# Kernel tuning notes

Hardware: AMD Instinct MI355X
Metric: run time of the kernel (lower is better)

## Reference

```python
import jax, jax.numpy as jnp
import numpy as np

B, DIM, H, W = 64, 640, 10, 10
EPS = 1e-05


def setup_inputs() -> dict:
    key = jax.random.key(0)
    k1, _ = jax.random.split(key)
    x = jax.random.normal(k1, (B, DIM, H, W), dtype=jnp.float32)
    init_temp = 1.0 / (2 * H * W)
    temperature = jnp.log(init_temp * jnp.ones((1, 1), dtype=jnp.float32))
    return {"x": x, "temperature": temperature}


def reference(x, temperature):
    b, d, h, w = x.shape
    xf = x.reshape(b, d, h * w)                       # [B, d, n]
    gram = jnp.einsum('bdn,ben->bde', xf, xf)         # [B, d, d]
    diag = jnp.diagonal(gram, axis1=1, axis2=2)       # [B, d]
    # ones @ (gram*eye) == diag[None,:]; (gram*eye) @ ones == diag[:,None]
    dcov = diag[:, :, None] + diag[:, None, :] - 2.0 * gram
    dcov = jnp.sqrt(jnp.exp(temperature[0, 0]) * jnp.clip(dcov, 0.0) + EPS)
    # double-centering: ones-matmuls are row/col/total means scaled by d
    row = jnp.mean(dcov, axis=2, keepdims=True)       # dcov @ ones / d
    col = jnp.mean(dcov, axis=1, keepdims=True)       # ones @ dcov / d
    tot = jnp.mean(dcov, axis=(1, 2), keepdims=True)  # ones @ dcov @ ones / d^2
    centered = dcov - row - col + tot                 # [B, d, d]
    iu = jnp.triu_indices(d)
    return centered[:, iu[0], iu[1]]                  # [B, d*(d+1)/2]
```

## Files before the change

kernel.cpp:

```cpp
#include <hip/hip_runtime.h>
#include <hip/hip_bf16.h>

#define B_    64
#define DIM   640
#define TS    64
#define NT    10
#define TRI   205120
#define EPS   1e-5f
#define SQEPS 3.1622776601683794e-3f
#define KCH   16
#define TILE_U4 1024
#define TILE_B  16384

typedef __attribute__((ext_vector_type(8)))  short bf16x8;
typedef __attribute__((ext_vector_type(16))) float f32x16;

__device__ inline unsigned pk_bf16(float a, float b) {
    __hip_bfloat162 h = __float22bfloat162_rn(float2{a, b});
    return *reinterpret_cast<unsigned*>(&h);
}
__device__ inline float bsq(unsigned pk) {
    union { unsigned u; float f; } a, c;
    a.u = pk << 16;
    c.u = pk & 0xffff0000u;
    return a.f * a.f + c.f * c.f;
}
__device__ inline float fsq(float x) { return __builtin_amdgcn_sqrtf(x); }

__device__ inline void gload_lds16(const void* g, void* l) {
    __builtin_amdgcn_global_load_lds(
        (const __attribute__((address_space(1))) unsigned*)g,
        (__attribute__((address_space(3))) unsigned*)l, 16, 0, 0);
}
__device__ inline void stage_tile16(const char* __restrict__ gt, char* lt,
                                    int wv, int lane) {
    #pragma unroll
    for (int it = 0; it < 4; ++it) {
        const int seg = (wv * 4 + it) * 1024;
        gload_lds16(gt + seg + lane * 16, lt + seg);
    }
}

__global__ __launch_bounds__(256) void prep_kernel(
    const float* __restrict__ x, uint4* __restrict__ img,
    float* __restrict__ dsq)
{
    const int blk = blockIdx.x;
    const int b = blk / NT, s = blk % NT;
    const int t = threadIdx.x;
    const float4* src = (const float4*)x + (size_t)(b * DIM + s * TS) * 25;
    uint4* dst = img + (size_t)blk * TILE_U4;

    #pragma unroll
    for (int ff = 0; ff < 4; ++ff) {
        const int f = t + ff * 256;
        const int r = f >> 4, c = f & 15;
        uint4 p = {0u, 0u, 0u, 0u};
        float sq = 0.f;
        if (c <= 12) {
            float4 lo = src[(size_t)r * 25 + 2 * c];
            float4 hi = make_float4(0.f, 0.f, 0.f, 0.f);
            if (c < 12) hi = src[(size_t)r * 25 + 2 * c + 1];
            p.x = pk_bf16(lo.x, lo.y);
            p.y = pk_bf16(lo.z, lo.w);
            p.z = pk_bf16(hi.x, hi.y);
            p.w = pk_bf16(hi.z, hi.w);
            sq = bsq(p.x) + bsq(p.y) + bsq(p.z) + bsq(p.w);
        }
        dst[r * KCH + (c ^ (r & 15))] = p;
        sq += __shfl_xor(sq, 1);
        sq += __shfl_xor(sq, 2);
        sq += __shfl_xor(sq, 4);
        sq += __shfl_xor(sq, 8);
        if (c == 0) dsq[b * DIM + s * TS + r] = sq;
    }
}

__global__ __launch_bounds__(256, 4) void strip_kernel(
    const uint4* __restrict__ img, const float* __restrict__ dsq,
    const float* __restrict__ temp, float* __restrict__ rowsum_part)
{
    __shared__ uint4 xj[2][TILE_U4];
    __shared__ float dAll[DIM];
    __shared__ float rpartw[2][TS];

    const int raw = blockIdx.x;
    const int bid = (raw & 7) * 160 + (raw >> 3);
    const int b = bid / 20, rem = bid % 20;
    const int s = rem >> 1, h = rem & 1;
    const int t = threadIdx.x, wv = t >> 6, lane = t & 63;
    const int l31 = lane & 31, khalf = lane >> 5;
    const int iq = wv & 1, jq = wv >> 1;
    const float tts = expf(temp[0]);
    const char* base = (const char*)(img + (size_t)b * NT * TILE_U4);

    stage_tile16(base + (size_t)h * TILE_B, (char*)xj[0], wv, lane);
    for (int k = t; k < DIM; k += 256) dAll[k] = dsq[b * DIM + k];

    const int irow = iq * 32 + l31;
    const uint4* own = img + (size_t)(b * NT + s) * TILE_U4;
    bf16x8 ifr[7];
    #pragma unroll
    for (int kk = 0; kk < 7; ++kk) {
        const int c = kk * 2 + khalf;
        ifr[kk] = *(const bf16x8*)&own[irow * KCH + (c ^ (irow & 15))];
    }
    const int jr = jq * 32 + l31;
    __syncthreads();
    const float dic = dAll[s * TS + irow];

    float rsum = 0.f;
    #pragma unroll
    for (int jj = 0; jj < 5; ++jj) {
        const int jt = h + 2 * jj;
        if (jj < 4)
            stage_tile16(base + (size_t)(jt + 2) * TILE_B,
                         (char*)xj[(jj + 1) & 1], wv, lane);
        const uint4* buf = xj[jj & 1];
        bf16x8 jfr[7];
        #pragma unroll
        for (int kk = 0; kk < 7; ++kk) {
            const int c = kk * 2 + khalf;
            jfr[kk] = *(const bf16x8*)&buf[jr * KCH + (c ^ (jr & 15))];
        }
        f32x16 acc = {};
        #pragma unroll
        for (int kk = 0; kk < 7; ++kk)
            acc = __builtin_amdgcn_mfma_f32_32x32x16_bf16(jfr[kk], ifr[kk],
                                                          acc, 0, 0, 0);
        const bool dg = (jt == s);
        #pragma unroll
        for (int r = 0; r < 16; ++r) {
            const int rf = (r & 3) + 8 * (r >> 2) + 4 * khalf;
            const int jrow = jq * 32 + rf;
            const float dj = dAll[jt * TS + jrow];
            float u = dj + dic - 2.f * acc[r];
            rsum += (dg && jrow == irow)
                  ? SQEPS : fsq(tts * fmaxf(u, 0.f) + EPS);
        }
        __syncthreads();
    }

    rsum += __shfl_xor(rsum, 32);
    if (lane < 32) rpartw[jq][iq * 32 + lane] = rsum;
    __syncthreads();
    if (t < TS)
        rowsum_part[h * (B_ * DIM) + b * DIM + s * TS + t]
            = rpartw[0][t] + rpartw[1][t];
}

__global__ __launch_bounds__(256, 4) void write_kernel(
    const uint4* __restrict__ img, const float* __restrict__ dsq,
    const float* __restrict__ temp, const float* __restrict__ rowsum_part,
    float* __restrict__ out)
{
    __shared__ uint4 xjb[2][TILE_U4];
    __shared__ float e[DIM];
    __shared__ float dAll[DIM];
    __shared__ float red4[4];

    const int raw = blockIdx.x;
    const int bid = (raw & 7) * 80 + (raw >> 3);
    const int b = bid / 10, rem = bid % 10;
    const int p = rem >> 1, h = rem & 1;
    const int t = threadIdx.x, wv = t >> 6, lane = t & 63;
    const int l31 = lane & 31, khalf = lane >> 5;
    const int wm = wv >> 1, wn = wv & 1;
    const float tts = expf(temp[0]);
    const char* base = (const char*)(img + (size_t)b * NT * TILE_U4);
    const float* r0 = rowsum_part + b * DIM;
    const float* r1 = rowsum_part + (B_ * DIM) + b * DIM;

    const int jf0 = p + ((p ^ h) & 1);
    stage_tile16(base + (size_t)jf0 * TILE_B, (char*)xjb[0], wv, lane);

    float ps = 0.f;
    for (int k = t; k < DIM; k += 256) {
        float rs = r0[k] + r1[k];
        e[k] = rs;
        dAll[k] = dsq[b * DIM + k];
        ps += rs;
    }
    ps += __shfl_xor(ps, 1);  ps += __shfl_xor(ps, 2);
    ps += __shfl_xor(ps, 4);  ps += __shfl_xor(ps, 8);
    ps += __shfl_xor(ps, 16); ps += __shfl_xor(ps, 32);
    if (lane == 0) red4[wv] = ps;
    __syncthreads();
    const float tm = (red4[0] + red4[1] + red4[2] + red4[3])
                   * (1.0f / ((float)DIM * (float)DIM));
    const float invD = 1.0f / (float)DIM;
    for (int k = t; k < DIM; k += 256)
        e[k] = 0.5f * tm - e[k] * invD;
    __syncthreads();

    const int arow = wm * 32 + l31;
    const int brow = wn * 32 + l31;

    #pragma unroll
    for (int si = 0; si < 2; ++si) {
        const int s = si ? (9 - p) : p;
        const int jf = s + ((s ^ h) & 1);
        if (jf >= NT) continue;
        if (si == 1) {
            stage_tile16(base + (size_t)jf * TILE_B, (char*)xjb[0], wv, lane);
            __syncthreads();
        }
        const int i0 = s * TS;
        const uint4* ownt = img + (size_t)(b * NT + s) * TILE_U4;
        bf16x8 afr[7];
        #pragma unroll
        for (int kk = 0; kk < 7; ++kk) {
            const int c = kk * 2 + khalf;
            afr[kk] = *(const bf16x8*)&ownt[arow * KCH + (c ^ (arow & 15))];
        }

        for (int j = jf, idx = 0; j < NT; j += 2, ++idx) {
            if (j + 2 < NT)
                stage_tile16(base + (size_t)(j + 2) * TILE_B,
                             (char*)xjb[(idx + 1) & 1], wv, lane);
            const uint4* buf = xjb[idx & 1];
            bf16x8 bfr7[7];
            #pragma unroll
            for (int kk = 0; kk < 7; ++kk) {
                const int c = kk * 2 + khalf;
                bfr7[kk] = *(const bf16x8*)&buf[brow * KCH + (c ^ (brow & 15))];
            }
            f32x16 acc = {};
            #pragma unroll
            for (int kk = 0; kk < 7; ++kk)
                acc = __builtin_amdgcn_mfma_f32_32x32x16_bf16(afr[kk], bfr7[kk],
                                                              acc, 0, 0, 0);
            const int j0 = j * TS;
            const int gj = j0 + brow;
            const float djc = dAll[gj], ejc = e[gj];
            #pragma unroll
            for (int g = 0; g < 4; ++g) {
                const int rbase = wm * 32 + 8 * g + 4 * khalf;
                const float4 e4 = *(const float4*)&e[i0 + rbase];
                const float4 d4 = *(const float4*)&dAll[i0 + rbase];
                #pragma unroll
                for (int q = 0; q < 4; ++q) {
                    const int r  = 4 * g + q;
                    const int gi = i0 + rbase + q;
                    float u = ((const float*)&d4)[q] + djc - 2.f * acc[r];
                    float v = (gi == gj) ? SQEPS
                                         : fsq(tts * fmaxf(u, 0.f) + EPS);
                    float cv = v + ((const float*)&e4)[q] + ejc;
                    const unsigned lo = (unsigned)min(gi, gj);
                    const unsigned hi2 = (unsigned)max(gi, gj);
                    unsigned idx32 = (unsigned)b * TRI + lo * DIM
                                   - ((lo * (lo - 1)) >> 1) - lo + hi2;
                    out[idx32] = cv;
                }
            }
            asm volatile("s_waitcnt vmcnt(16)" ::: "memory");
            __builtin_amdgcn_sched_barrier(0);
            __builtin_amdgcn_s_barrier();
        }
    }
}

extern "C" void kernel_launch(void* const* d_in, const int* in_sizes, int n_in,
                              void* d_out, int out_size, void* d_ws, size_t ws_size,
                              hipStream_t stream)
{
    const float* x    = (const float*)d_in[0];
    const float* temp = (const float*)d_in[1];
    float* out         = (float*)d_out;

    float* rowsum_part = (float*)d_ws;
    float* dsq         = rowsum_part + 2 * B_ * DIM;
    uint4* img         = (uint4*)(dsq + B_ * DIM);

    prep_kernel <<<B_ * NT,     256, 0, stream>>>(x, img, dsq);
    strip_kernel<<<2 * B_ * NT, 256, 0, stream>>>(img, dsq, temp, rowsum_part);
    write_kernel<<<B_ * NT,     256, 0, stream>>>(img, dsq, temp, rowsum_part, out);
}
```

Before: 47.44 us.

## Split write kernel into per-tile-pair blocks with separate means kernel

The per-batch centering terms (row means and total mean) move into a new small means_kernel that writes them to workspace. The write kernel is restructured from persistent blocks that loop over several j-tiles with double-buffered staging into one block per upper-triangular tile pair (55 per batch). This raises parallelism and drops the in-block reduction and pipelining, at the cost of an extra kernel launch and more redundant tile staging per block.

```diff
diff --git a/kernel.cpp b/kernel.cpp
--- a/kernel.cpp
+++ b/kernel.cpp
@@ -5,6 +5,7 @@
 #define DIM   640
 #define TS    64
 #define NT    10
+#define NTP   55
 #define TRI   205120
 #define EPS   1e-5f
 #define SQEPS 3.1622776601683794e-3f
@@ -149,38 +150,19 @@
             = rpartw[0][t] + rpartw[1][t];
 }
 
-__global__ __launch_bounds__(256, 4) void write_kernel(
-    const uint4* __restrict__ img, const float* __restrict__ dsq,
-    const float* __restrict__ temp, const float* __restrict__ rowsum_part,
-    float* __restrict__ out)
-{
-    __shared__ uint4 xjb[2][TILE_U4];
-    __shared__ float e[DIM];
-    __shared__ float dAll[DIM];
+__global__ __launch_bounds__(256) void means_kernel(
+    const float* __restrict__ rowsum_part, float* __restrict__ e_g)
+{
     __shared__ float red4[4];
-
-    const int raw = blockIdx.x;
-    const int bid = (raw & 7) * 80 + (raw >> 3);
-    const int b = bid / 10, rem = bid % 10;
-    const int p = rem >> 1, h = rem & 1;
-    const int t = threadIdx.x, wv = t >> 6, lane = t & 63;
-    const int l31 = lane & 31, khalf = lane >> 5;
-    const int wm = wv >> 1, wn = wv & 1;
-    const float tts = expf(temp[0]);
-    const char* base = (const char*)(img + (size_t)b * NT * TILE_U4);
+    const int b = blockIdx.x, t = threadIdx.x;
+    const int wv = t >> 6, lane = t & 63;
     const float* r0 = rowsum_part + b * DIM;
     const float* r1 = rowsum_part + (B_ * DIM) + b * DIM;
 
-    const int jf0 = p + ((p ^ h) & 1);
-    stage_tile16(base + (size_t)jf0 * TILE_B, (char*)xjb[0], wv, lane);
-
-    float ps = 0.f;
-    for (int k = t; k < DIM; k += 256) {
-        float rs = r0[k] + r1[k];
-        e[k] = rs;
-        dAll[k] = dsq[b * DIM + k];
-        ps += rs;
-    }
+    const float v0 = r0[t] + r1[t];
+    const float v1 = r0[t + 256] + r1[t + 256];
+    const float v2 = (t < 128) ? (r0[t + 512] + r1[t + 512]) : 0.f;
+    float ps = v0 + v1 + v2;
     ps += __shfl_xor(ps, 1);  ps += __shfl_xor(ps, 2);
     ps += __shfl_xor(ps, 4);  ps += __shfl_xor(ps, 8);
     ps += __shfl_xor(ps, 16); ps += __shfl_xor(ps, 32);
@@ -189,73 +171,84 @@
     const float tm = (red4[0] + red4[1] + red4[2] + red4[3])
                    * (1.0f / ((float)DIM * (float)DIM));
     const float invD = 1.0f / (float)DIM;
-    for (int k = t; k < DIM; k += 256)
-        e[k] = 0.5f * tm - e[k] * invD;
-    __syncthreads();
-
+    e_g[b * DIM + t]       = 0.5f * tm - v0 * invD;
+    e_g[b * DIM + t + 256] = 0.5f * tm - v1 * invD;
+    if (t < 128)
+        e_g[b * DIM + t + 512] = 0.5f * tm - v2 * invD;
+}
+
+__device__ inline void decode_blk(int raw, int& b, int& ti, int& tj) {
+    int bid = (raw & 7) * (B_ * NTP / 8) + (raw >> 3);
+    b = bid / NTP;
+    int tp = bid % NTP;
+    int i = 0;
+    while (tp >= NT - i) { tp -= NT - i; ++i; }
+    ti = i; tj = i + tp;
+}
+
+__global__ __launch_bounds__(256, 4) void write_kernel(
+    const uint4* __restrict__ img, const float* __restrict__ dsq,
+    const float* __restrict__ temp, const float* __restrict__ e_g,
+    float* __restrict__ out)
+{
+    __shared__ uint4 xi[TILE_U4], xj2[TILE_U4];
+    __shared__ float dIs[TS], dJs[TS], eIs[TS], eJs[TS];
+
+    int b, ti, tj; decode_blk(blockIdx.x, b, ti, tj);
+    const int t = threadIdx.x, wv = t >> 6, lane = t & 63;
+    const int l31 = lane & 31, khalf = lane >> 5;
+    const int wm = wv >> 1, wn = wv & 1;
+    const int i0 = ti * TS, j0 = tj * TS;
+    const float tts = expf(temp[0]);
+    const char* base = (const char*)(img + (size_t)b * NT * TILE_U4);
+
+    stage_tile16(base + (size_t)ti * TILE_B, (char*)xi, wv, lane);
+    if (ti != tj)
+        stage_tile16(base + (size_t)tj * TILE_B, (char*)xj2, wv, lane);
+
+    if      (t < TS)     dIs[t]          = dsq[b * DIM + i0 + t];
+    else if (t < 2 * TS) dJs[t - TS]     = dsq[b * DIM + j0 + (t - TS)];
+    else if (t < 3 * TS) eIs[t - 2 * TS] = e_g[b * DIM + i0 + (t - 2 * TS)];
+    else                 eJs[t - 3 * TS] = e_g[b * DIM + j0 + (t - 3 * TS)];
+    __syncthreads();
+
+    const uint4* xjp = (ti == tj) ? xi : xj2;
     const int arow = wm * 32 + l31;
     const int brow = wn * 32 + l31;
 
-    #pragma unroll
-    for (int si = 0; si < 2; ++si) {
-        const int s = si ? (9 - p) : p;
-        const int jf = s + ((s ^ h) & 1);
-        if (jf >= NT) continue;
-        if (si == 1) {
-            stage_tile16(base + (size_t)jf * TILE_B, (char*)xjb[0], wv, lane);
-            __syncthreads();
-        }
-        const int i0 = s * TS;
-        const uint4* ownt = img + (size_t)(b * NT + s) * TILE_U4;
-        bf16x8 afr[7];
-        #pragma unroll
-        for (int kk = 0; kk < 7; ++kk) {
-            const int c = kk * 2 + khalf;
-            afr[kk] = *(const bf16x8*)&ownt[arow * KCH + (c ^ (arow & 15))];
-        }
-
-        for (int j = jf, idx = 0; j < NT; j += 2, ++idx) {
-            if (j + 2 < NT)
-                stage_tile16(base + (size_t)(j + 2) * TILE_B,
-                             (char*)xjb[(idx + 1) & 1], wv, lane);
-            const uint4* buf = xjb[idx & 1];
-            bf16x8 bfr7[7];
-            #pragma unroll
-            for (int kk = 0; kk < 7; ++kk) {
-                const int c = kk * 2 + khalf;
-                bfr7[kk] = *(const bf16x8*)&buf[brow * KCH + (c ^ (brow & 15))];
-            }
-            f32x16 acc = {};
-            #pragma unroll
-            for (int kk = 0; kk < 7; ++kk)
-                acc = __builtin_amdgcn_mfma_f32_32x32x16_bf16(afr[kk], bfr7[kk],
-                                                              acc, 0, 0, 0);
-            const int j0 = j * TS;
-            const int gj = j0 + brow;
-            const float djc = dAll[gj], ejc = e[gj];
-            #pragma unroll
-            for (int g = 0; g < 4; ++g) {
-                const int rbase = wm * 32 + 8 * g + 4 * khalf;
-                const float4 e4 = *(const float4*)&e[i0 + rbase];
-                const float4 d4 = *(const float4*)&dAll[i0 + rbase];
-                #pragma unroll
-                for (int q = 0; q < 4; ++q) {
-                    const int r  = 4 * g + q;
-                    const int gi = i0 + rbase + q;
-                    float u = ((const float*)&d4)[q] + djc - 2.f * acc[r];
-                    float v = (gi == gj) ? SQEPS
-                                         : fsq(tts * fmaxf(u, 0.f) + EPS);
-                    float cv = v + ((const float*)&e4)[q] + ejc;
-                    const unsigned lo = (unsigned)min(gi, gj);
-                    const unsigned hi2 = (unsigned)max(gi, gj);
-                    unsigned idx32 = (unsigned)b * TRI + lo * DIM
-                                   - ((lo * (lo - 1)) >> 1) - lo + hi2;
-                    out[idx32] = cv;
-                }
-            }
-            asm volatile("s_waitcnt vmcnt(16)" ::: "memory");
-            __builtin_amdgcn_sched_barrier(0);
-            __builtin_amdgcn_s_barrier();
+    bf16x8 afr[7], bfr7[7];
+    #pragma unroll
+    for (int kk = 0; kk < 7; ++kk) {
+        const int c = kk * 2 + khalf;
+        afr[kk]  = *(const bf16x8*)&xi[arow * KCH + (c ^ (arow & 15))];
+        bfr7[kk] = *(const bf16x8*)&xjp[brow * KCH + (c ^ (brow & 15))];
+    }
+    f32x16 acc = {};
+    #pragma unroll
+    for (int kk = 0; kk < 7; ++kk)
+        acc = __builtin_amdgcn_mfma_f32_32x32x16_bf16(afr[kk], bfr7[kk],
+                                                      acc, 0, 0, 0);
+
+    const int col_l = wn * 32 + l31;
+    const int gj = j0 + col_l;
+    const float djc = dJs[col_l], ejc = eJs[col_l];
+    #pragma unroll
+    for (int g = 0; g < 4; ++g) {
+        const int rbase = wm * 32 + 8 * g + 4 * khalf;
+        const float4 e4 = *(const float4*)&eIs[rbase];
+        const float4 d4 = *(const float4*)&dIs[rbase];
+        #pragma unroll
+        for (int q = 0; q < 4; ++q) {
+            const int r  = 4 * g + q;
+            const int gi = i0 + rbase + q;
+            float u = ((const float*)&d4)[q] + djc - 2.f * acc[r];
+            float v = (gi == gj) ? SQEPS : fsq(tts * fmaxf(u, 0.f) + EPS);
+            float cv = v + ((const float*)&e4)[q] + ejc;
+            const unsigned lo = (unsigned)min(gi, gj);
+            const unsigned hi2 = (unsigned)max(gi, gj);
+            unsigned idx32 = (unsigned)b * TRI + lo * DIM
+                           - ((lo * (lo - 1)) >> 1) - lo + hi2;
+            out[idx32] = cv;
         }
     }
 }
@@ -270,9 +263,11 @@
 
     float* rowsum_part = (float*)d_ws;
     float* dsq         = rowsum_part + 2 * B_ * DIM;
-    uint4* img         = (uint4*)(dsq + B_ * DIM);
+    float* e_g         = dsq + B_ * DIM;
+    uint4* img         = (uint4*)(e_g + B_ * DIM);
 
     prep_kernel <<<B_ * NT,     256, 0, stream>>>(x, img, dsq);
     strip_kernel<<<2 * B_ * NT, 256, 0, stream>>>(img, dsq, temp, rowsum_part);
-    write_kernel<<<B_ * NT,     256, 0, stream>>>(img, dsq, temp, rowsum_part, out);
-}
+    means_kernel<<<B_,          256, 0, stream>>>(rowsum_part, e_g);
+    write_kernel<<<B_ * NTP,    256, 0, stream>>>(img, dsq, temp, e_g, out);
+}
```

Measured after the change: 45.96 us (median of 2 runs). 3.1% less time.
